# Kernel optimization log

Measured on AMD Instinct MI355X. Metric: run time of the kernel, lower is better.

Reference implementation:

```python
import jax, jax.numpy as jnp
import numpy as np

WH = WW = 7          # window size
N_TOK = WH * WW      # 49 tokens per window
HEADS = 8
HEAD_DIM = 32
DIM = HEADS * HEAD_DIM  # 256
NW = 64              # windows per image (56x56 / 7x7)
BW = 64 * NW         # batch_images * windows = 4096


def _rel_pos_index(wh, ww):
    # Swin-style relative position index, flattened to (N*N,)
    coords = np.stack(np.meshgrid(np.arange(wh), np.arange(ww), indexing='ij'))  # (2, wh, ww)
    coords = coords.reshape(2, -1)                                               # (2, N)
    rel = coords[:, :, None] - coords[:, None, :]                                # (2, N, N)
    rel = rel.transpose(1, 2, 0).astype(np.int64)                                # (N, N, 2)
    rel[:, :, 0] += wh - 1
    rel[:, :, 1] += ww - 1
    rel[:, :, 0] *= 2 * ww - 1
    return jnp.asarray(rel.sum(-1).reshape(-1))                                  # (N*N,)

_REL_IDX = _rel_pos_index(WH, WW)


def setup_inputs() -> dict:
    key = jax.random.key(0)
    ks = jax.random.split(key, 5)
    x = jax.random.normal(ks[0], (BW, N_TOK, DIM), dtype=jnp.float32)
    mask = jnp.zeros((1, NW, 1, N_TOK, N_TOK), dtype=jnp.float32)
    w_qkv = jax.random.normal(ks[1], (DIM, 3 * HEADS * HEAD_DIM), dtype=jnp.float32) * 0.02
    b_qkv = jnp.zeros((3 * HEADS * HEAD_DIM,), dtype=jnp.float32)
    rel_table = jax.random.normal(ks[2], ((2 * WH - 1) * (2 * WW - 1), HEADS), dtype=jnp.float32) * 0.02
    w_out = jax.random.normal(ks[3], (HEADS * HEAD_DIM, DIM), dtype=jnp.float32) * 0.02
    b_out = jnp.zeros((DIM,), dtype=jnp.float32)
    return {"x": x, "mask": mask, "w_qkv": w_qkv, "b_qkv": b_qkv,
            "rel_table": rel_table, "w_out": w_out, "b_out": b_out}


def reference(x, mask, w_qkv, b_qkv, rel_table, w_out, b_out):
    bw, n, d = x.shape
    # QKV projection then split per original Rearrange:
    # 'b n (qkv h hd) -> qkv b h n hd'
    qkv = (x @ w_qkv + b_qkv).reshape(bw, n, 3, HEADS, HEAD_DIM)
    qkv = qkv.transpose(2, 0, 3, 1, 4)  # (3, bw, h, n, hd)
    q, k, v = qkv[0], qkv[1], qkv[2]
    # NOTE: original computes einsum('bnid,bnjd->bnij', k, q): a[i,j] = k_i . q_j
    a = jnp.einsum('bhid,bhjd->bhij', k, q) / jnp.sqrt(jnp.asarray(HEAD_DIM, x.dtype))
    # relative position bias: table gather then '(i j) h -> h i j'
    bias = rel_table[_REL_IDX].reshape(n, n, HEADS).transpose(2, 0, 1)  # (h, n, n)
    a = a + bias
    # mask add: '(b nW) h i j -> b nW h i j', + mask, back
    nw = mask.shape[1]
    a = a.reshape(bw // nw, nw, HEADS, n, n) + mask
    a = a.reshape(bw, HEADS, n, n)
    a = jax.nn.softmax(a, axis=-1)
    y = jnp.einsum('bhij,bhjd->bhid', a, v)        # (bw, h, n, hd)
    y = y.transpose(0, 2, 1, 3).reshape(bw, n, HEADS * HEAD_DIM)
    return y @ w_out + b_out
```

## Files before the change

kernel.cpp:

```cpp
#include <hip/hip_runtime.h>

typedef __attribute__((ext_vector_type(8))) short short8;
typedef __attribute__((ext_vector_type(4))) float f32x4;
typedef unsigned short u16;

#define NTOK 49
#define NBLK 4096
#define LOG2E 1.4426950408889634f

#define XF 0
#define VY 16384
#define POOLN 32768

#define WS_WQT 0
#define WS_WOT 393216
#define WS_BIAS 524288
#define WS_MKG 655360

__device__ __forceinline__ u16 f2bf(float f) {
  unsigned u = __float_as_uint(f);
  return (u16)((u + 0x7fffu + ((u >> 16) & 1u)) >> 16);
}
__device__ __forceinline__ unsigned packbf(float a, float b) {
  unsigned r;
  asm("v_cvt_pk_bf16_f32 %0, %1, %2" : "=v"(r) : "v"(a), "v"(b));
  return r;
}

__device__ __forceinline__ short8 asm_frag(unsigned c0p0, unsigned c0p1,
                                           unsigned c1p0, unsigned c1p1,
                                           int srcA, int srcB, bool cSel) {
  unsigned a0 = (unsigned)__shfl((int)c0p0, srcA);
  unsigned b0 = (unsigned)__shfl((int)c1p0, srcA);
  unsigned a1 = (unsigned)__shfl((int)c0p1, srcA);
  unsigned b1 = (unsigned)__shfl((int)c1p1, srcA);
  unsigned a2 = (unsigned)__shfl((int)c0p0, srcB);
  unsigned b2 = (unsigned)__shfl((int)c1p0, srcB);
  unsigned a3 = (unsigned)__shfl((int)c0p1, srcB);
  unsigned b3 = (unsigned)__shfl((int)c1p1, srcB);
  union { unsigned u[4]; short8 s8; } r;
  r.u[0] = cSel ? b0 : a0;
  r.u[1] = cSel ? b1 : a1;
  r.u[2] = cSel ? b2 : a2;
  r.u[3] = cSel ? b3 : a3;
  return r.s8;
}

__global__ void prep_kernel(const float* __restrict__ w_qkv,
                            const float* __restrict__ w_out,
                            const float* __restrict__ rel,
                            const float* __restrict__ mask,
                            u16* __restrict__ wqTf,
                            u16* __restrict__ woTf,
                            float* __restrict__ biasf,
                            float* __restrict__ mkg) {
  const int stride = gridDim.x * blockDim.x;
  const int gid = blockIdx.x * blockDim.x + threadIdx.x;
  for (int e = gid; e < 48 * 8 * 64 * 8; e += stride) {
    int eL = e & 7, ln = (e >> 3) & 63, ks = (e >> 9) & 7, ctg = e >> 12;
    int k = ks * 32 + (ln >> 4) * 8 + eL;
    int c = ctg * 16 + (ln & 15);
    wqTf[e] = f2bf(w_qkv[k * 768 + c]);
  }
  for (int e = gid; e < 16 * 8 * 64 * 8; e += stride) {
    int eL = e & 7, ln = (e >> 3) & 63, ks = (e >> 9) & 7, ctg = e >> 12;
    int k = ks * 32 + (ln >> 4) * 8 + eL;
    int c = ctg * 16 + (ln & 15);
    woTf[e] = f2bf(w_out[k * 256 + c]);
  }
  for (int e = gid; e < 8 * 16 * 64 * 4; e += stride) {
    int rg = e & 3, ln = (e >> 2) & 63, t = (e >> 8) & 15, hh = e >> 12;
    int i = (t >> 2) * 16 + (ln & 15);
    int j = (t & 3) * 16 + (ln >> 4) * 4 + rg;
    float v;
    if (j >= NTOK) v = -1e30f;
    else if (i >= NTOK) v = 0.f;
    else {
      int dh = i / 7 - j / 7 + 6;
      int dw = i % 7 - j % 7 + 6;
      v = rel[(dh * 13 + dw) * 8 + hh];
    }
    biasf[e] = v * LOG2E;
  }
  for (int e = gid; e < 64 * 16 * 64 * 4; e += stride) {
    int rg = e & 3, ln = (e >> 2) & 63, t = (e >> 8) & 15, wdw = e >> 12;
    int i = (t >> 2) * 16 + (ln & 15);
    int j = (t & 3) * 16 + (ln >> 4) * 4 + rg;
    mkg[e] = (i < NTOK && j < NTOK) ? mask[wdw * (NTOK * NTOK) + i * NTOK + j] * LOG2E : 0.f;
  }
}

__global__ void __launch_bounds__(512, 2) winattn_mfma(
    const float* __restrict__ x,
    const float* __restrict__ b_qkv,
    const float* __restrict__ b_out,
    const u16* __restrict__ wqTf,
    const u16* __restrict__ woTf,
    const float* __restrict__ biasf,
    const float* __restrict__ mkg,
    float* __restrict__ out)
{
  __shared__ u16 pool[POOLN];
  const int b = blockIdx.x, tid = threadIdx.x;
  const int lane = tid & 63, lo = lane & 15, hi = lane >> 4;
  const int h = tid >> 6;
  const f32x4 zf = {0.f, 0.f, 0.f, 0.f};

  {
    const float4* xg = (const float4*)(x + (size_t)b * (NTOK * 256));
    for (int e = tid; e < 49 * 64; e += 512) {
      float4 v = xg[e];
      int r = e >> 6, c4 = (e & 63) << 2;
      int addr = (((r >> 4) * 8 + (c4 >> 5)) * 64 + ((c4 >> 3) & 3) * 16 + (r & 15)) * 8 + (c4 & 7);
      *(uint2*)&pool[XF + addr] = make_uint2(packbf(v.x, v.y), packbf(v.z, v.w));
    }
    if (tid < 15 * 64) {
      int e = tid;
      int r = 49 + (e >> 6), c4 = (e & 63) << 2;
      int addr = (((r >> 4) * 8 + (c4 >> 5)) * 64 + ((c4 >> 3) & 3) * 16 + (r & 15)) * 8 + (c4 & 7);
      *(uint2*)&pool[XF + addr] = make_uint2(0u, 0u);
    }
  }
  __syncthreads();

  const int srcA = lo + 32 * (hi & 1);
  const int srcB = srcA + 16;
  const bool cSel = (hi & 2) != 0;

  short8 qa[4], ka[4];
  {
    unsigned pq[2][4][2];
    {
      f32x4 acc[2][4];
      #pragma unroll
      for (int ct = 0; ct < 2; ++ct)
        #pragma unroll
        for (int rt = 0; rt < 4; ++rt) acc[ct][rt] = zf;
      #pragma unroll
      for (int ks = 0; ks < 8; ++ks) {
        short8 bx[4];
        #pragma unroll
        for (int rt = 0; rt < 4; ++rt)
          bx[rt] = *(const short8*)&pool[XF + ((rt * 8 + ks) * 64 + lane) * 8];
        short8 af0 = *(const short8*)&wqTf[((size_t)((2 * h) * 8 + ks) * 64 + lane) * 8];
        short8 af1 = *(const short8*)&wqTf[((size_t)((2 * h + 1) * 8 + ks) * 64 + lane) * 8];
        #pragma unroll
        for (int rt = 0; rt < 4; ++rt) {
          acc[0][rt] = __builtin_amdgcn_mfma_f32_16x16x32_bf16(af0, bx[rt], acc[0][rt], 0, 0, 0);
          acc[1][rt] = __builtin_amdgcn_mfma_f32_16x16x32_bf16(af1, bx[rt], acc[1][rt], 0, 0, 0);
        }
      }
      #pragma unroll
      for (int ct = 0; ct < 2; ++ct) {
        f32x4 bias = *(const f32x4*)(b_qkv + (2 * h + ct) * 16 + hi * 4);
        #pragma unroll
        for (int rt = 0; rt < 4; ++rt) {
          f32x4 v = acc[ct][rt] + bias;
          pq[ct][rt][0] = packbf(v[0], v[1]);
          pq[ct][rt][1] = packbf(v[2], v[3]);
        }
      }
    }
    {
      f32x4 acc[2][4];
      #pragma unroll
      for (int ct = 0; ct < 2; ++ct)
        #pragma unroll
        for (int rt = 0; rt < 4; ++rt) acc[ct][rt] = zf;
      #pragma unroll
      for (int ks = 0; ks < 8; ++ks) {
        short8 bx[4];
        #pragma unroll
        for (int rt = 0; rt < 4; ++rt)
          bx[rt] = *(const short8*)&pool[XF + ((rt * 8 + ks) * 64 + lane) * 8];
        short8 af0 = *(const short8*)&wqTf[((size_t)((16 + 2 * h) * 8 + ks) * 64 + lane) * 8];
        short8 af1 = *(const short8*)&wqTf[((size_t)((17 + 2 * h) * 8 + ks) * 64 + lane) * 8];
        #pragma unroll
        for (int rt = 0; rt < 4; ++rt) {
          acc[0][rt] = __builtin_amdgcn_mfma_f32_16x16x32_bf16(af0, bx[rt], acc[0][rt], 0, 0, 0);
          acc[1][rt] = __builtin_amdgcn_mfma_f32_16x16x32_bf16(af1, bx[rt], acc[1][rt], 0, 0, 0);
        }
      }
      unsigned pk[2][4][2];
      #pragma unroll
      for (int ct = 0; ct < 2; ++ct) {
        f32x4 bias = *(const f32x4*)(b_qkv + (16 + 2 * h + ct) * 16 + hi * 4);
        #pragma unroll
        for (int rt = 0; rt < 4; ++rt) {
          f32x4 v = acc[ct][rt] + bias;
          pk[ct][rt][0] = packbf(v[0], v[1]);
          pk[ct][rt][1] = packbf(v[2], v[3]);
        }
      }
      #pragma unroll
      for (int it = 0; it < 4; ++it)
        ka[it] = asm_frag(pk[0][it][0], pk[0][it][1], pk[1][it][0], pk[1][it][1],
                          srcA, srcB, cSel);
    }
    {
      f32x4 acc[2][4];
      #pragma unroll
      for (int ct = 0; ct < 2; ++ct)
        #pragma unroll
        for (int rt = 0; rt < 4; ++rt) acc[ct][rt] = zf;
      #pragma unroll
      for (int ks = 0; ks < 8; ++ks) {
        short8 bx[4];
        #pragma unroll
        for (int rt = 0; rt < 4; ++rt)
          bx[rt] = *(const short8*)&pool[XF + ((rt * 8 + ks) * 64 + lane) * 8];
        short8 af0 = *(const short8*)&wqTf[((size_t)((32 + 2 * h) * 8 + ks) * 64 + lane) * 8];
        short8 af1 = *(const short8*)&wqTf[((size_t)((33 + 2 * h) * 8 + ks) * 64 + lane) * 8];
        #pragma unroll
        for (int rt = 0; rt < 4; ++rt) {
          acc[0][rt] = __builtin_amdgcn_mfma_f32_16x16x32_bf16(bx[rt], af0, acc[0][rt], 0, 0, 0);
          acc[1][rt] = __builtin_amdgcn_mfma_f32_16x16x32_bf16(bx[rt], af1, acc[1][rt], 0, 0, 0);
        }
      }
      #pragma unroll
      for (int ct = 0; ct < 2; ++ct) {
        const float bv = b_qkv[(32 + 2 * h + ct) * 16 + lo];
        #pragma unroll
        for (int rt = 0; rt < 4; ++rt) {
          f32x4 v = acc[ct][rt];
          float v0 = v[0] + bv, v1 = v[1] + bv, v2 = v[2] + bv, v3 = v[3] + bv;
          int f = ct * 2 + (rt >> 1);
          int hiR = (rt & 1) * 2 + (hi >> 1);
          int eb = (hi & 1) * 4;
          *(uint2*)&pool[VY + (f * 8 + h) * 512 + (hiR * 16 + lo) * 8 + eb] =
              make_uint2(packbf(v0, v1), packbf(v2, v3));
        }
      }
    }
    #pragma unroll
    for (int jt = 0; jt < 4; ++jt)
      qa[jt] = asm_frag(pq[0][jt][0], pq[0][jt][1], pq[1][jt][0], pq[1][jt][1],
                        srcA, srcB, cSel);
  }
  __syncthreads();

  {
    short8 va[2][2];
    #pragma unroll
    for (int dblk = 0; dblk < 2; ++dblk)
      #pragma unroll
      for (int k2 = 0; k2 < 2; ++k2)
        va[dblk][k2] = *(const short8*)&pool[VY + ((dblk * 2 + k2) * 8 + h) * 512 + lane * 8];
    const float SC = 0.17677669529663687f * LOG2E;
    const float* bh = biasf + h * 4096;
    const float* mh = mkg + (size_t)(b & 63) * 4096;
    #pragma unroll
    for (int it = 0; it < 4; ++it) {
      float rs = 0.f;
      unsigned pit[4][2];
      #pragma unroll
      for (int jt = 0; jt < 4; ++jt) {
        f32x4 s = __builtin_amdgcn_mfma_f32_16x16x32_bf16(qa[jt], ka[it], zf, 0, 0, 0);
        const int t = it * 4 + jt;
        f32x4 bm = *(const f32x4*)&bh[(t * 64 + lane) * 4];
        f32x4 mm = *(const f32x4*)&mh[(t * 64 + lane) * 4];
        float p0 = exp2f(fmaf(s[0], SC, bm[0] + mm[0]));
        float p1 = exp2f(fmaf(s[1], SC, bm[1] + mm[1]));
        float p2 = exp2f(fmaf(s[2], SC, bm[2] + mm[2]));
        float p3 = exp2f(fmaf(s[3], SC, bm[3] + mm[3]));
        rs += (p0 + p1) + (p2 + p3);
        pit[jt][0] = packbf(p0, p1);
        pit[jt][1] = packbf(p2, p3);
      }
      float r2 = rs + __shfl_xor(rs, 16);
      const float inv = 1.f / (r2 + __shfl_xor(r2, 32));
      f32x4 ya0 = zf, ya1 = zf;
      #pragma unroll
      for (int k2 = 0; k2 < 2; ++k2) {
        short8 pb = asm_frag(pit[2 * k2][0], pit[2 * k2][1],
                             pit[2 * k2 + 1][0], pit[2 * k2 + 1][1], srcA, srcB, cSel);
        ya0 = __builtin_amdgcn_mfma_f32_16x16x32_bf16(va[0][k2], pb, ya0, 0, 0, 0);
        ya1 = __builtin_amdgcn_mfma_f32_16x16x32_bf16(va[1][k2], pb, ya1, 0, 0, 0);
      }
      #pragma unroll
      for (int dblk = 0; dblk < 2; ++dblk) {
        f32x4 yy = dblk ? ya1 : ya0;
        int hi2 = dblk * 2 + (hi >> 1);
        int eb = (hi & 1) * 4;
        *(uint2*)&pool[XF + ((it * 8 + h) * 64 + hi2 * 16 + lo) * 8 + eb] =
            make_uint2(packbf(yy[0] * inv, yy[1] * inv), packbf(yy[2] * inv, yy[3] * inv));
      }
    }
  }
  __syncthreads();

  {
    f32x4 pacc[2][4];
    #pragma unroll
    for (int ct = 0; ct < 2; ++ct)
      #pragma unroll
      for (int rt = 0; rt < 4; ++rt) pacc[ct][rt] = zf;
    #pragma unroll
    for (int ks = 0; ks < 8; ++ks) {
      short8 yb[4];
      #pragma unroll
      for (int rt = 0; rt < 4; ++rt)
        yb[rt] = *(const short8*)&pool[XF + ((rt * 8 + ks) * 64 + lane) * 8];
      #pragma unroll
      for (int ct = 0; ct < 2; ++ct) {
        short8 wf = *(const short8*)&woTf[((size_t)((h * 2 + ct) * 8 + ks) * 64 + lane) * 8];
        #pragma unroll
        for (int rt = 0; rt < 4; ++rt)
          pacc[ct][rt] = __builtin_amdgcn_mfma_f32_16x16x32_bf16(wf, yb[rt], pacc[ct][rt], 0, 0, 0);
      }
    }
    float* og = out + (size_t)b * (NTOK * 256);
    #pragma unroll
    for (int ct = 0; ct < 2; ++ct) {
      const int cb = (h * 2 + ct) * 16 + hi * 4;
      f32x4 bb = *(const f32x4*)(b_out + cb);
      #pragma unroll
      for (int rt = 0; rt < 4; ++rt) {
        const int r = rt * 16 + lo;
        if (r < NTOK) {
          f32x4 vv = pacc[ct][rt] + bb;
          *(f32x4*)(og + (size_t)r * 256 + cb) = vv;
        }
      }
    }
  }
}

extern "C" void kernel_launch(void* const* d_in, const int* in_sizes, int n_in,
                              void* d_out, int out_size, void* d_ws, size_t ws_size,
                              hipStream_t stream) {
  const float *x = nullptr, *mask = nullptr, *w_qkv = nullptr, *b_qkv = nullptr,
              *rel_t = nullptr, *w_out = nullptr, *b_out = nullptr;
  for (int i = 0; i < n_in; ++i) {
    const float* p = (const float*)d_in[i];
    switch (in_sizes[i]) {
      case 4096 * 49 * 256: x = p; break;
      case 64 * 49 * 49:    mask = p; break;
      case 256 * 768:       w_qkv = p; break;
      case 768:             b_qkv = p; break;
      case 169 * 8:         rel_t = p; break;
      case 256 * 256:       w_out = p; break;
      case 256:             b_out = p; break;
    }
  }
  char* wsb = (char*)d_ws;
  u16* wqTf    = (u16*)(wsb + WS_WQT);
  u16* woTf    = (u16*)(wsb + WS_WOT);
  float* biasf = (float*)(wsb + WS_BIAS);
  float* mkg   = (float*)(wsb + WS_MKG);

  hipLaunchKernelGGL(prep_kernel, dim3(1024), dim3(256), 0, stream,
                     w_qkv, w_out, rel_t, mask, wqTf, woTf, biasf, mkg);
  hipLaunchKernelGGL(winattn_mfma, dim3(NBLK), dim3(512), 0, stream,
                     x, b_qkv, b_out, wqTf, woTf, biasf, mkg, (float*)d_out);
}
```

Measured before the change: 343.3 us.

## Process two windows per 1024-thread block and route P through LDS

Each block now runs 1024 threads as two independent 512-thread groups, each handling one window with its own half of a doubled LDS pool. The launch bound changes from (512,2) to (1024,1), and the grid halves to 2048 blocks. The Q, K and V projections are restructured into separate top-level scopes, likely to cut live ranges. The P fragment for the PV matmul is now written to LDS and read back instead of being built in registers with asm_frag. That reuses the V region, which looks hazardous: V fragments are loaded into registers first, so a stale read may be fine, but the P writes and reads have no barrier within the wave. The extra LDS traffic and the tighter occupancy constraint could offset any gain.

```diff
diff --git a/kernel.cpp b/kernel.cpp
--- a/kernel.cpp
+++ b/kernel.cpp
@@ -5,12 +5,12 @@
 typedef unsigned short u16;
 
 #define NTOK 49
-#define NBLK 4096
 #define LOG2E 1.4426950408889634f
 
 #define XF 0
 #define VY 16384
-#define POOLN 32768
+#define GP 32768
+#define POOLN 65536
 
 #define WS_WQT 0
 #define WS_WOT 393216
@@ -90,7 +90,7 @@
   }
 }
 
-__global__ void __launch_bounds__(512, 2) winattn_mfma(
+__global__ void __launch_bounds__(1024, 1) winattn_mfma(
     const float* __restrict__ x,
     const float* __restrict__ b_qkv,
     const float* __restrict__ b_out,
@@ -101,24 +101,28 @@
     float* __restrict__ out)
 {
   __shared__ u16 pool[POOLN];
-  const int b = blockIdx.x, tid = threadIdx.x;
-  const int lane = tid & 63, lo = lane & 15, hi = lane >> 4;
-  const int h = tid >> 6;
+  const int tid = threadIdx.x;
+  const int g = tid >> 9;
+  const int gtid = tid & 511;
+  const int lane = gtid & 63, lo = lane & 15, hi = lane >> 4;
+  const int h = gtid >> 6;
+  const int b2 = blockIdx.x * 2 + g;
+  u16* gp = pool + g * GP;
   const f32x4 zf = {0.f, 0.f, 0.f, 0.f};
 
   {
-    const float4* xg = (const float4*)(x + (size_t)b * (NTOK * 256));
-    for (int e = tid; e < 49 * 64; e += 512) {
+    const float4* xg = (const float4*)(x + (size_t)b2 * (NTOK * 256));
+    for (int e = gtid; e < 49 * 64; e += 512) {
       float4 v = xg[e];
       int r = e >> 6, c4 = (e & 63) << 2;
       int addr = (((r >> 4) * 8 + (c4 >> 5)) * 64 + ((c4 >> 3) & 3) * 16 + (r & 15)) * 8 + (c4 & 7);
-      *(uint2*)&pool[XF + addr] = make_uint2(packbf(v.x, v.y), packbf(v.z, v.w));
-    }
-    if (tid < 15 * 64) {
-      int e = tid;
+      *(uint2*)&gp[XF + addr] = make_uint2(packbf(v.x, v.y), packbf(v.z, v.w));
+    }
+    if (gtid < 15 * 64) {
+      int e = gtid;
       int r = 49 + (e >> 6), c4 = (e & 63) << 2;
       int addr = (((r >> 4) * 8 + (c4 >> 5)) * 64 + ((c4 >> 3) & 3) * 16 + (r & 15)) * 8 + (c4 & 7);
-      *(uint2*)&pool[XF + addr] = make_uint2(0u, 0u);
+      *(uint2*)&gp[XF + addr] = make_uint2(0u, 0u);
     }
   }
   __syncthreads();
@@ -129,107 +133,34 @@
 
   short8 qa[4], ka[4];
   {
+    f32x4 acc[2][4];
+    #pragma unroll
+    for (int ct = 0; ct < 2; ++ct)
+      #pragma unroll
+      for (int rt = 0; rt < 4; ++rt) acc[ct][rt] = zf;
+    #pragma unroll
+    for (int ks = 0; ks < 8; ++ks) {
+      short8 bx[4];
+      #pragma unroll
+      for (int rt = 0; rt < 4; ++rt)
+        bx[rt] = *(const short8*)&gp[XF + ((rt * 8 + ks) * 64 + lane) * 8];
+      short8 af0 = *(const short8*)&wqTf[((size_t)((2 * h) * 8 + ks) * 64 + lane) * 8];
+      short8 af1 = *(const short8*)&wqTf[((size_t)((2 * h + 1) * 8 + ks) * 64 + lane) * 8];
+      #pragma unroll
+      for (int rt = 0; rt < 4; ++rt) {
+        acc[0][rt] = __builtin_amdgcn_mfma_f32_16x16x32_bf16(af0, bx[rt], acc[0][rt], 0, 0, 0);
+        acc[1][rt] = __builtin_amdgcn_mfma_f32_16x16x32_bf16(af1, bx[rt], acc[1][rt], 0, 0, 0);
+      }
+    }
     unsigned pq[2][4][2];
-    {
-      f32x4 acc[2][4];
-      #pragma unroll
-      for (int ct = 0; ct < 2; ++ct)
-        #pragma unroll
-        for (int rt = 0; rt < 4; ++rt) acc[ct][rt] = zf;
-      #pragma unroll
-      for (int ks = 0; ks < 8; ++ks) {
-        short8 bx[4];
-        #pragma unroll
-        for (int rt = 0; rt < 4; ++rt)
-          bx[rt] = *(const short8*)&pool[XF + ((rt * 8 + ks) * 64 + lane) * 8];
-        short8 af0 = *(const short8*)&wqTf[((size_t)((2 * h) * 8 + ks) * 64 + lane) * 8];
-        short8 af1 = *(const short8*)&wqTf[((size_t)((2 * h + 1) * 8 + ks) * 64 + lane) * 8];
-        #pragma unroll
-        for (int rt = 0; rt < 4; ++rt) {
-          acc[0][rt] = __builtin_amdgcn_mfma_f32_16x16x32_bf16(af0, bx[rt], acc[0][rt], 0, 0, 0);
-          acc[1][rt] = __builtin_amdgcn_mfma_f32_16x16x32_bf16(af1, bx[rt], acc[1][rt], 0, 0, 0);
-        }
-      }
-      #pragma unroll
-      for (int ct = 0; ct < 2; ++ct) {
-        f32x4 bias = *(const f32x4*)(b_qkv + (2 * h + ct) * 16 + hi * 4);
-        #pragma unroll
-        for (int rt = 0; rt < 4; ++rt) {
-          f32x4 v = acc[ct][rt] + bias;
-          pq[ct][rt][0] = packbf(v[0], v[1]);
-          pq[ct][rt][1] = packbf(v[2], v[3]);
-        }
-      }
-    }
-    {
-      f32x4 acc[2][4];
-      #pragma unroll
-      for (int ct = 0; ct < 2; ++ct)
-        #pragma unroll
-        for (int rt = 0; rt < 4; ++rt) acc[ct][rt] = zf;
-      #pragma unroll
-      for (int ks = 0; ks < 8; ++ks) {
-        short8 bx[4];
-        #pragma unroll
-        for (int rt = 0; rt < 4; ++rt)
-          bx[rt] = *(const short8*)&pool[XF + ((rt * 8 + ks) * 64 + lane) * 8];
-        short8 af0 = *(const short8*)&wqTf[((size_t)((16 + 2 * h) * 8 + ks) * 64 + lane) * 8];
-        short8 af1 = *(const short8*)&wqTf[((size_t)((17 + 2 * h) * 8 + ks) * 64 + lane) * 8];
-        #pragma unroll
-        for (int rt = 0; rt < 4; ++rt) {
-          acc[0][rt] = __builtin_amdgcn_mfma_f32_16x16x32_bf16(af0, bx[rt], acc[0][rt], 0, 0, 0);
-          acc[1][rt] = __builtin_amdgcn_mfma_f32_16x16x32_bf16(af1, bx[rt], acc[1][rt], 0, 0, 0);
-        }
-      }
-      unsigned pk[2][4][2];
-      #pragma unroll
-      for (int ct = 0; ct < 2; ++ct) {
-        f32x4 bias = *(const f32x4*)(b_qkv + (16 + 2 * h + ct) * 16 + hi * 4);
-        #pragma unroll
-        for (int rt = 0; rt < 4; ++rt) {
-          f32x4 v = acc[ct][rt] + bias;
-          pk[ct][rt][0] = packbf(v[0], v[1]);
-          pk[ct][rt][1] = packbf(v[2], v[3]);
-        }
-      }
-      #pragma unroll
-      for (int it = 0; it < 4; ++it)
-        ka[it] = asm_frag(pk[0][it][0], pk[0][it][1], pk[1][it][0], pk[1][it][1],
-                          srcA, srcB, cSel);
-    }
-    {
-      f32x4 acc[2][4];
-      #pragma unroll
-      for (int ct = 0; ct < 2; ++ct)
-        #pragma unroll
-        for (int rt = 0; rt < 4; ++rt) acc[ct][rt] = zf;
-      #pragma unroll
-      for (int ks = 0; ks < 8; ++ks) {
-        short8 bx[4];
-        #pragma unroll
-        for (int rt = 0; rt < 4; ++rt)
-          bx[rt] = *(const short8*)&pool[XF + ((rt * 8 + ks) * 64 + lane) * 8];
-        short8 af0 = *(const short8*)&wqTf[((size_t)((32 + 2 * h) * 8 + ks) * 64 + lane) * 8];
-        short8 af1 = *(const short8*)&wqTf[((size_t)((33 + 2 * h) * 8 + ks) * 64 + lane) * 8];
-        #pragma unroll
-        for (int rt = 0; rt < 4; ++rt) {
-          acc[0][rt] = __builtin_amdgcn_mfma_f32_16x16x32_bf16(bx[rt], af0, acc[0][rt], 0, 0, 0);
-          acc[1][rt] = __builtin_amdgcn_mfma_f32_16x16x32_bf16(bx[rt], af1, acc[1][rt], 0, 0, 0);
-        }
-      }
-      #pragma unroll
-      for (int ct = 0; ct < 2; ++ct) {
-        const float bv = b_qkv[(32 + 2 * h + ct) * 16 + lo];
-        #pragma unroll
-        for (int rt = 0; rt < 4; ++rt) {
-          f32x4 v = acc[ct][rt];
-          float v0 = v[0] + bv, v1 = v[1] + bv, v2 = v[2] + bv, v3 = v[3] + bv;
-          int f = ct * 2 + (rt >> 1);
-          int hiR = (rt & 1) * 2 + (hi >> 1);
-          int eb = (hi & 1) * 4;
-          *(uint2*)&pool[VY + (f * 8 + h) * 512 + (hiR * 16 + lo) * 8 + eb] =
-              make_uint2(packbf(v0, v1), packbf(v2, v3));
-        }
+    #pragma unroll
+    for (int ct = 0; ct < 2; ++ct) {
+      f32x4 bias = *(const f32x4*)(b_qkv + (2 * h + ct) * 16 + hi * 4);
+      #pragma unroll
+      for (int rt = 0; rt < 4; ++rt) {
+        f32x4 v = acc[ct][rt] + bias;
+        pq[ct][rt][0] = packbf(v[0], v[1]);
+        pq[ct][rt][1] = packbf(v[2], v[3]);
       }
     }
     #pragma unroll
@@ -237,6 +168,77 @@
       qa[jt] = asm_frag(pq[0][jt][0], pq[0][jt][1], pq[1][jt][0], pq[1][jt][1],
                         srcA, srcB, cSel);
   }
+  {
+    f32x4 acc[2][4];
+    #pragma unroll
+    for (int ct = 0; ct < 2; ++ct)
+      #pragma unroll
+      for (int rt = 0; rt < 4; ++rt) acc[ct][rt] = zf;
+    #pragma unroll
+    for (int ks = 0; ks < 8; ++ks) {
+      short8 bx[4];
+      #pragma unroll
+      for (int rt = 0; rt < 4; ++rt)
+        bx[rt] = *(const short8*)&gp[XF + ((rt * 8 + ks) * 64 + lane) * 8];
+      short8 af0 = *(const short8*)&wqTf[((size_t)((16 + 2 * h) * 8 + ks) * 64 + lane) * 8];
+      short8 af1 = *(const short8*)&wqTf[((size_t)((17 + 2 * h) * 8 + ks) * 64 + lane) * 8];
+      #pragma unroll
+      for (int rt = 0; rt < 4; ++rt) {
+        acc[0][rt] = __builtin_amdgcn_mfma_f32_16x16x32_bf16(af0, bx[rt], acc[0][rt], 0, 0, 0);
+        acc[1][rt] = __builtin_amdgcn_mfma_f32_16x16x32_bf16(af1, bx[rt], acc[1][rt], 0, 0, 0);
+      }
+    }
+    unsigned pk[2][4][2];
+    #pragma unroll
+    for (int ct = 0; ct < 2; ++ct) {
+      f32x4 bias = *(const f32x4*)(b_qkv + (16 + 2 * h + ct) * 16 + hi * 4);
+      #pragma unroll
+      for (int rt = 0; rt < 4; ++rt) {
+        f32x4 v = acc[ct][rt] + bias;
+        pk[ct][rt][0] = packbf(v[0], v[1]);
+        pk[ct][rt][1] = packbf(v[2], v[3]);
+      }
+    }
+    #pragma unroll
+    for (int it = 0; it < 4; ++it)
+      ka[it] = asm_frag(pk[0][it][0], pk[0][it][1], pk[1][it][0], pk[1][it][1],
+                        srcA, srcB, cSel);
+  }
+  {
+    f32x4 acc[2][4];
+    #pragma unroll
+    for (int ct = 0; ct < 2; ++ct)
+      #pragma unroll
+      for (int rt = 0; rt < 4; ++rt) acc[ct][rt] = zf;
+    #pragma unroll
+    for (int ks = 0; ks < 8; ++ks) {
+      short8 bx[4];
+      #pragma unroll
+      for (int rt = 0; rt < 4; ++rt)
+        bx[rt] = *(const short8*)&gp[XF + ((rt * 8 + ks) * 64 + lane) * 8];
+      short8 af0 = *(const short8*)&wqTf[((size_t)((32 + 2 * h) * 8 + ks) * 64 + lane) * 8];
+      short8 af1 = *(const short8*)&wqTf[((size_t)((33 + 2 * h) * 8 + ks) * 64 + lane) * 8];
+      #pragma unroll
+      for (int rt = 0; rt < 4; ++rt) {
+        acc[0][rt] = __builtin_amdgcn_mfma_f32_16x16x32_bf16(bx[rt], af0, acc[0][rt], 0, 0, 0);
+        acc[1][rt] = __builtin_amdgcn_mfma_f32_16x16x32_bf16(bx[rt], af1, acc[1][rt], 0, 0, 0);
+      }
+    }
+    #pragma unroll
+    for (int ct = 0; ct < 2; ++ct) {
+      const float bv = b_qkv[(32 + 2 * h + ct) * 16 + lo];
+      #pragma unroll
+      for (int rt = 0; rt < 4; ++rt) {
+        f32x4 v = acc[ct][rt];
+        float v0 = v[0] + bv, v1 = v[1] + bv, v2 = v[2] + bv, v3 = v[3] + bv;
+        int f = ct * 2 + (rt >> 1);
+        int hiR = (rt & 1) * 2 + (hi >> 1);
+        int eb = (hi & 1) * 4;
+        *(uint2*)&gp[VY + (f * 8 + h) * 512 + (hiR * 16 + lo) * 8 + eb] =
+            make_uint2(packbf(v0, v1), packbf(v2, v3));
+      }
+    }
+  }
   __syncthreads();
 
   {
@@ -245,10 +247,10 @@
     for (int dblk = 0; dblk < 2; ++dblk)
       #pragma unroll
       for (int k2 = 0; k2 < 2; ++k2)
-        va[dblk][k2] = *(const short8*)&pool[VY + ((dblk * 2 + k2) * 8 + h) * 512 + lane * 8];
+        va[dblk][k2] = *(const short8*)&gp[VY + ((dblk * 2 + k2) * 8 + h) * 512 + lane * 8];
     const float SC = 0.17677669529663687f * LOG2E;
     const float* bh = biasf + h * 4096;
-    const float* mh = mkg + (size_t)(b & 63) * 4096;
+    const float* mh = mkg + (size_t)(b2 & 63) * 4096;
     #pragma unroll
     for (int it = 0; it < 4; ++it) {
       float rs = 0.f;
@@ -267,13 +269,20 @@
         pit[jt][0] = packbf(p0, p1);
         pit[jt][1] = packbf(p2, p3);
       }
+      #pragma unroll
+      for (int jt = 0; jt < 4; ++jt) {
+        int k2 = jt >> 1;
+        int hi2 = (jt & 1) * 2 + (hi >> 1);
+        int eb = (hi & 1) * 4;
+        *(uint2*)&gp[VY + (k2 * 8 + h) * 512 + (hi2 * 16 + lo) * 8 + eb] =
+            make_uint2(pit[jt][0], pit[jt][1]);
+      }
       float r2 = rs + __shfl_xor(rs, 16);
       const float inv = 1.f / (r2 + __shfl_xor(r2, 32));
       f32x4 ya0 = zf, ya1 = zf;
       #pragma unroll
       for (int k2 = 0; k2 < 2; ++k2) {
-        short8 pb = asm_frag(pit[2 * k2][0], pit[2 * k2][1],
-                             pit[2 * k2 + 1][0], pit[2 * k2 + 1][1], srcA, srcB, cSel);
+        short8 pb = *(const short8*)&gp[VY + (k2 * 8 + h) * 512 + lane * 8];
         ya0 = __builtin_amdgcn_mfma_f32_16x16x32_bf16(va[0][k2], pb, ya0, 0, 0, 0);
         ya1 = __builtin_amdgcn_mfma_f32_16x16x32_bf16(va[1][k2], pb, ya1, 0, 0, 0);
       }
@@ -282,7 +291,7 @@
         f32x4 yy = dblk ? ya1 : ya0;
         int hi2 = dblk * 2 + (hi >> 1);
         int eb = (hi & 1) * 4;
-        *(uint2*)&pool[XF + ((it * 8 + h) * 64 + hi2 * 16 + lo) * 8 + eb] =
+        *(uint2*)&gp[XF + ((it * 8 + h) * 64 + hi2 * 16 + lo) * 8 + eb] =
             make_uint2(packbf(yy[0] * inv, yy[1] * inv), packbf(yy[2] * inv, yy[3] * inv));
       }
     }
@@ -300,7 +309,7 @@
       short8 yb[4];
       #pragma unroll
       for (int rt = 0; rt < 4; ++rt)
-        yb[rt] = *(const short8*)&pool[XF + ((rt * 8 + ks) * 64 + lane) * 8];
+        yb[rt] = *(const short8*)&gp[XF + ((rt * 8 + ks) * 64 + lane) * 8];
       #pragma unroll
       for (int ct = 0; ct < 2; ++ct) {
         short8 wf = *(const short8*)&woTf[((size_t)((h * 2 + ct) * 8 + ks) * 64 + lane) * 8];
@@ -309,7 +318,7 @@
           pacc[ct][rt] = __builtin_amdgcn_mfma_f32_16x16x32_bf16(wf, yb[rt], pacc[ct][rt], 0, 0, 0);
       }
     }
-    float* og = out + (size_t)b * (NTOK * 256);
+    float* og = out + (size_t)b2 * (NTOK * 256);
     #pragma unroll
     for (int ct = 0; ct < 2; ++ct) {
       const int cb = (h * 2 + ct) * 16 + hi * 4;
@@ -351,6 +360,6 @@
 
   hipLaunchKernelGGL(prep_kernel, dim3(1024), dim3(256), 0, stream,
                      w_qkv, w_out, rel_t, mask, wqTf, woTf, biasf, mkg);
-  hipLaunchKernelGGL(winattn_mfma, dim3(NBLK), dim3(512), 0, stream,
+  hipLaunchKernelGGL(winattn_mfma, dim3(2048), dim3(1024), 0, stream,
                      x, b_qkv, b_out, wqTf, woTf, biasf, mkg, (float*)d_out);
 }
```

Measured after the change: 646.9 us. 88.4% more time.

## Fold softmax scale into Q weights, precombine bias+mask, use LDS for fragment transposes

Applied to the files above, without the earlier changes.

Pre-scales the Q projection weights and bias by 1/sqrt(d)*log2e so the score FMA becomes a plain add. An extra prep kernel builds a combined per-window, per-head bias+mask table (8 MB), so each score tile needs one global load instead of two. The shuffle-based fragment transposes for Q, K and P are replaced with LDS round-trips, and the Y layout in LDS is changed. This trades cross-lane shuffles for LDS traffic and adds one syncthreads, a larger combined table that must stay cached, and a launch that depends on workspace size.

```diff
diff --git a/kernel.cpp b/kernel.cpp
--- a/kernel.cpp
+++ b/kernel.cpp
@@ -14,8 +14,11 @@
 
 #define WS_WQT 0
 #define WS_WOT 393216
-#define WS_BIAS 524288
-#define WS_MKG 655360
+#define WS_BQS 524288
+#define WS_BIAS 528384
+#define WS_MKG 659456
+#define WS_CMB 1708032
+#define WS_NEED (WS_CMB + 8388608)
 
 __device__ __forceinline__ u16 f2bf(float f) {
   unsigned u = __float_as_uint(f);
@@ -27,40 +30,26 @@
   return r;
 }
 
-__device__ __forceinline__ short8 asm_frag(unsigned c0p0, unsigned c0p1,
-                                           unsigned c1p0, unsigned c1p1,
-                                           int srcA, int srcB, bool cSel) {
-  unsigned a0 = (unsigned)__shfl((int)c0p0, srcA);
-  unsigned b0 = (unsigned)__shfl((int)c1p0, srcA);
-  unsigned a1 = (unsigned)__shfl((int)c0p1, srcA);
-  unsigned b1 = (unsigned)__shfl((int)c1p1, srcA);
-  unsigned a2 = (unsigned)__shfl((int)c0p0, srcB);
-  unsigned b2 = (unsigned)__shfl((int)c1p0, srcB);
-  unsigned a3 = (unsigned)__shfl((int)c0p1, srcB);
-  unsigned b3 = (unsigned)__shfl((int)c1p1, srcB);
-  union { unsigned u[4]; short8 s8; } r;
-  r.u[0] = cSel ? b0 : a0;
-  r.u[1] = cSel ? b1 : a1;
-  r.u[2] = cSel ? b2 : a2;
-  r.u[3] = cSel ? b3 : a3;
-  return r.s8;
-}
-
 __global__ void prep_kernel(const float* __restrict__ w_qkv,
                             const float* __restrict__ w_out,
                             const float* __restrict__ rel,
                             const float* __restrict__ mask,
+                            const float* __restrict__ b_qkv,
                             u16* __restrict__ wqTf,
                             u16* __restrict__ woTf,
+                            float* __restrict__ bqs,
                             float* __restrict__ biasf,
                             float* __restrict__ mkg) {
+  const float SCQ = 0.17677669529663687f * LOG2E;
   const int stride = gridDim.x * blockDim.x;
   const int gid = blockIdx.x * blockDim.x + threadIdx.x;
   for (int e = gid; e < 48 * 8 * 64 * 8; e += stride) {
     int eL = e & 7, ln = (e >> 3) & 63, ks = (e >> 9) & 7, ctg = e >> 12;
     int k = ks * 32 + (ln >> 4) * 8 + eL;
     int c = ctg * 16 + (ln & 15);
-    wqTf[e] = f2bf(w_qkv[k * 768 + c]);
+    float wv = w_qkv[k * 768 + c];
+    if (ctg < 16) wv *= SCQ;
+    wqTf[e] = f2bf(wv);
   }
   for (int e = gid; e < 16 * 8 * 64 * 8; e += stride) {
     int eL = e & 7, ln = (e >> 3) & 63, ks = (e >> 9) & 7, ctg = e >> 12;
@@ -68,6 +57,8 @@
     int c = ctg * 16 + (ln & 15);
     woTf[e] = f2bf(w_out[k * 256 + c]);
   }
+  for (int e = gid; e < 768; e += stride)
+    bqs[e] = b_qkv[e] * (e < 256 ? SCQ : 1.f);
   for (int e = gid; e < 8 * 16 * 64 * 4; e += stride) {
     int rg = e & 3, ln = (e >> 2) & 63, t = (e >> 8) & 15, hh = e >> 12;
     int i = (t >> 2) * 16 + (ln & 15);
@@ -90,14 +81,25 @@
   }
 }
 
+__global__ void prep2_kernel(const float* __restrict__ biasf,
+                             const float* __restrict__ mkg,
+                             float* __restrict__ cmb) {
+  const int stride = gridDim.x * blockDim.x;
+  for (int e = blockIdx.x * blockDim.x + threadIdx.x; e < 64 * 8 * 4096; e += stride) {
+    int x = e & 4095, hh = (e >> 12) & 7, wdw = e >> 15;
+    cmb[e] = biasf[hh * 4096 + x] + mkg[wdw * 4096 + x];
+  }
+}
+
 __global__ void __launch_bounds__(512, 2) winattn_mfma(
     const float* __restrict__ x,
-    const float* __restrict__ b_qkv,
+    const float* __restrict__ bqs,
     const float* __restrict__ b_out,
     const u16* __restrict__ wqTf,
     const u16* __restrict__ woTf,
     const float* __restrict__ biasf,
     const float* __restrict__ mkg,
+    const float* __restrict__ cmb,
     float* __restrict__ out)
 {
   __shared__ u16 pool[POOLN];
@@ -114,8 +116,7 @@
       int addr = (((r >> 4) * 8 + (c4 >> 5)) * 64 + ((c4 >> 3) & 3) * 16 + (r & 15)) * 8 + (c4 & 7);
       *(uint2*)&pool[XF + addr] = make_uint2(packbf(v.x, v.y), packbf(v.z, v.w));
     }
-    if (tid < 15 * 64) {
-      int e = tid;
+    for (int e = tid; e < 15 * 64; e += 512) {
       int r = 49 + (e >> 6), c4 = (e & 63) << 2;
       int addr = (((r >> 4) * 8 + (c4 >> 5)) * 64 + ((c4 >> 3) & 3) * 16 + (r & 15)) * 8 + (c4 & 7);
       *(uint2*)&pool[XF + addr] = make_uint2(0u, 0u);
@@ -123,103 +124,52 @@
   }
   __syncthreads();
 
-  const int srcA = lo + 32 * (hi & 1);
-  const int srcB = srcA + 16;
-  const bool cSel = (hi & 2) != 0;
-
-  short8 qa[4], ka[4];
-  {
-    unsigned pq[2][4][2];
-    {
-      f32x4 acc[2][4];
-      #pragma unroll
-      for (int ct = 0; ct < 2; ++ct)
-        #pragma unroll
-        for (int rt = 0; rt < 4; ++rt) acc[ct][rt] = zf;
-      #pragma unroll
-      for (int ks = 0; ks < 8; ++ks) {
-        short8 bx[4];
-        #pragma unroll
-        for (int rt = 0; rt < 4; ++rt)
-          bx[rt] = *(const short8*)&pool[XF + ((rt * 8 + ks) * 64 + lane) * 8];
-        short8 af0 = *(const short8*)&wqTf[((size_t)((2 * h) * 8 + ks) * 64 + lane) * 8];
-        short8 af1 = *(const short8*)&wqTf[((size_t)((2 * h + 1) * 8 + ks) * 64 + lane) * 8];
+  unsigned pq[2][4][2], pk[2][4][2];
+  #pragma unroll
+  for (int pass = 0; pass < 3; ++pass) {
+    const int c0 = (pass == 0) ? 2 * h : (pass == 1 ? 16 + 2 * h : 32 + 2 * h);
+    f32x4 acc[2][4];
+    #pragma unroll
+    for (int ct = 0; ct < 2; ++ct)
+      #pragma unroll
+      for (int rt = 0; rt < 4; ++rt) acc[ct][rt] = zf;
+    #pragma unroll
+    for (int ks = 0; ks < 8; ++ks) {
+      short8 bx[4];
+      #pragma unroll
+      for (int rt = 0; rt < 4; ++rt)
+        bx[rt] = *(const short8*)&pool[XF + ((rt * 8 + ks) * 64 + lane) * 8];
+      short8 af0 = *(const short8*)&wqTf[((size_t)((c0 + 0) * 8 + ks) * 64 + lane) * 8];
+      short8 af1 = *(const short8*)&wqTf[((size_t)((c0 + 1) * 8 + ks) * 64 + lane) * 8];
+      if (pass < 2) {
         #pragma unroll
         for (int rt = 0; rt < 4; ++rt) {
           acc[0][rt] = __builtin_amdgcn_mfma_f32_16x16x32_bf16(af0, bx[rt], acc[0][rt], 0, 0, 0);
           acc[1][rt] = __builtin_amdgcn_mfma_f32_16x16x32_bf16(af1, bx[rt], acc[1][rt], 0, 0, 0);
         }
-      }
-      #pragma unroll
-      for (int ct = 0; ct < 2; ++ct) {
-        f32x4 bias = *(const f32x4*)(b_qkv + (2 * h + ct) * 16 + hi * 4);
-        #pragma unroll
-        for (int rt = 0; rt < 4; ++rt) {
-          f32x4 v = acc[ct][rt] + bias;
-          pq[ct][rt][0] = packbf(v[0], v[1]);
-          pq[ct][rt][1] = packbf(v[2], v[3]);
-        }
-      }
-    }
-    {
-      f32x4 acc[2][4];
-      #pragma unroll
-      for (int ct = 0; ct < 2; ++ct)
-        #pragma unroll
-        for (int rt = 0; rt < 4; ++rt) acc[ct][rt] = zf;
-      #pragma unroll
-      for (int ks = 0; ks < 8; ++ks) {
-        short8 bx[4];
-        #pragma unroll
-        for (int rt = 0; rt < 4; ++rt)
-          bx[rt] = *(const short8*)&pool[XF + ((rt * 8 + ks) * 64 + lane) * 8];
-        short8 af0 = *(const short8*)&wqTf[((size_t)((16 + 2 * h) * 8 + ks) * 64 + lane) * 8];
-        short8 af1 = *(const short8*)&wqTf[((size_t)((17 + 2 * h) * 8 + ks) * 64 + lane) * 8];
-        #pragma unroll
-        for (int rt = 0; rt < 4; ++rt) {
-          acc[0][rt] = __builtin_amdgcn_mfma_f32_16x16x32_bf16(af0, bx[rt], acc[0][rt], 0, 0, 0);
-          acc[1][rt] = __builtin_amdgcn_mfma_f32_16x16x32_bf16(af1, bx[rt], acc[1][rt], 0, 0, 0);
-        }
-      }
-      unsigned pk[2][4][2];
-      #pragma unroll
-      for (int ct = 0; ct < 2; ++ct) {
-        f32x4 bias = *(const f32x4*)(b_qkv + (16 + 2 * h + ct) * 16 + hi * 4);
-        #pragma unroll
-        for (int rt = 0; rt < 4; ++rt) {
-          f32x4 v = acc[ct][rt] + bias;
-          pk[ct][rt][0] = packbf(v[0], v[1]);
-          pk[ct][rt][1] = packbf(v[2], v[3]);
-        }
-      }
-      #pragma unroll
-      for (int it = 0; it < 4; ++it)
-        ka[it] = asm_frag(pk[0][it][0], pk[0][it][1], pk[1][it][0], pk[1][it][1],
-                          srcA, srcB, cSel);
-    }
-    {
-      f32x4 acc[2][4];
-      #pragma unroll
-      for (int ct = 0; ct < 2; ++ct)
-        #pragma unroll
-        for (int rt = 0; rt < 4; ++rt) acc[ct][rt] = zf;
-      #pragma unroll
-      for (int ks = 0; ks < 8; ++ks) {
-        short8 bx[4];
-        #pragma unroll
-        for (int rt = 0; rt < 4; ++rt)
-          bx[rt] = *(const short8*)&pool[XF + ((rt * 8 + ks) * 64 + lane) * 8];
-        short8 af0 = *(const short8*)&wqTf[((size_t)((32 + 2 * h) * 8 + ks) * 64 + lane) * 8];
-        short8 af1 = *(const short8*)&wqTf[((size_t)((33 + 2 * h) * 8 + ks) * 64 + lane) * 8];
+      } else {
         #pragma unroll
         for (int rt = 0; rt < 4; ++rt) {
           acc[0][rt] = __builtin_amdgcn_mfma_f32_16x16x32_bf16(bx[rt], af0, acc[0][rt], 0, 0, 0);
           acc[1][rt] = __builtin_amdgcn_mfma_f32_16x16x32_bf16(bx[rt], af1, acc[1][rt], 0, 0, 0);
         }
       }
+    }
+    if (pass < 2) {
       #pragma unroll
       for (int ct = 0; ct < 2; ++ct) {
-        const float bv = b_qkv[(32 + 2 * h + ct) * 16 + lo];
+        f32x4 bias = *(const f32x4*)(bqs + (c0 + ct) * 16 + hi * 4);
+        #pragma unroll
+        for (int rt = 0; rt < 4; ++rt) {
+          f32x4 v = acc[ct][rt] + bias;
+          if (pass == 0) { pq[ct][rt][0] = packbf(v[0], v[1]); pq[ct][rt][1] = packbf(v[2], v[3]); }
+          else           { pk[ct][rt][0] = packbf(v[0], v[1]); pk[ct][rt][1] = packbf(v[2], v[3]); }
+        }
+      }
+    } else {
+      #pragma unroll
+      for (int ct = 0; ct < 2; ++ct) {
+        const float bv = bqs[(c0 + ct) * 16 + lo];
         #pragma unroll
         for (int rt = 0; rt < 4; ++rt) {
           f32x4 v = acc[ct][rt];
@@ -232,12 +182,37 @@
         }
       }
     }
+  }
+  __syncthreads();
+
+  short8 qa[4], ka[4];
+  {
+    u16* slice = pool + XF + h * 2048;
+    #pragma unroll
+    for (int ct = 0; ct < 2; ++ct)
+      #pragma unroll
+      for (int rt = 0; rt < 4; ++rt) {
+        int hi2 = ct * 2 + (hi >> 1);
+        int eb = (hi & 1) * 4;
+        *(uint2*)&slice[(rt * 64 + hi2 * 16 + lo) * 8 + eb] =
+            make_uint2(pq[ct][rt][0], pq[ct][rt][1]);
+      }
     #pragma unroll
     for (int jt = 0; jt < 4; ++jt)
-      qa[jt] = asm_frag(pq[0][jt][0], pq[0][jt][1], pq[1][jt][0], pq[1][jt][1],
-                        srcA, srcB, cSel);
-  }
-  __syncthreads();
+      qa[jt] = *(const short8*)&slice[(jt * 64 + lane) * 8];
+    #pragma unroll
+    for (int ct = 0; ct < 2; ++ct)
+      #pragma unroll
+      for (int rt = 0; rt < 4; ++rt) {
+        int hi2 = ct * 2 + (hi >> 1);
+        int eb = (hi & 1) * 4;
+        *(uint2*)&slice[(rt * 64 + hi2 * 16 + lo) * 8 + eb] =
+            make_uint2(pk[ct][rt][0], pk[ct][rt][1]);
+      }
+    #pragma unroll
+    for (int it = 0; it < 4; ++it)
+      ka[it] = *(const short8*)&slice[(it * 64 + lane) * 8];
+  }
 
   {
     short8 va[2][2];
@@ -246,34 +221,43 @@
       #pragma unroll
       for (int k2 = 0; k2 < 2; ++k2)
         va[dblk][k2] = *(const short8*)&pool[VY + ((dblk * 2 + k2) * 8 + h) * 512 + lane * 8];
-    const float SC = 0.17677669529663687f * LOG2E;
-    const float* bh = biasf + h * 4096;
-    const float* mh = mkg + (size_t)(b & 63) * 4096;
+    const float* cb;
+    const float* mb = nullptr;
+    if (cmb) {
+      cb = cmb + (((size_t)(b & 63) * 8 + h) << 12);
+    } else {
+      cb = biasf + h * 4096;
+      mb = mkg + (size_t)(b & 63) * 4096;
+    }
     #pragma unroll
     for (int it = 0; it < 4; ++it) {
       float rs = 0.f;
-      unsigned pit[4][2];
       #pragma unroll
       for (int jt = 0; jt < 4; ++jt) {
         f32x4 s = __builtin_amdgcn_mfma_f32_16x16x32_bf16(qa[jt], ka[it], zf, 0, 0, 0);
         const int t = it * 4 + jt;
-        f32x4 bm = *(const f32x4*)&bh[(t * 64 + lane) * 4];
-        f32x4 mm = *(const f32x4*)&mh[(t * 64 + lane) * 4];
-        float p0 = exp2f(fmaf(s[0], SC, bm[0] + mm[0]));
-        float p1 = exp2f(fmaf(s[1], SC, bm[1] + mm[1]));
-        float p2 = exp2f(fmaf(s[2], SC, bm[2] + mm[2]));
-        float p3 = exp2f(fmaf(s[3], SC, bm[3] + mm[3]));
+        f32x4 c4 = *(const f32x4*)&cb[(t * 64 + lane) * 4];
+        if (mb) {
+          f32x4 m4 = *(const f32x4*)&mb[(t * 64 + lane) * 4];
+          c4[0] += m4[0]; c4[1] += m4[1]; c4[2] += m4[2]; c4[3] += m4[3];
+        }
+        float p0 = exp2f(s[0] + c4[0]);
+        float p1 = exp2f(s[1] + c4[1]);
+        float p2 = exp2f(s[2] + c4[2]);
+        float p3 = exp2f(s[3] + c4[3]);
         rs += (p0 + p1) + (p2 + p3);
-        pit[jt][0] = packbf(p0, p1);
-        pit[jt][1] = packbf(p2, p3);
+        int k2 = jt >> 1;
+        int hi2 = (jt & 1) * 2 + (hi >> 1);
+        int eb = (hi & 1) * 4;
+        *(uint2*)&pool[VY + (k2 * 8 + h) * 512 + (hi2 * 16 + lo) * 8 + eb] =
+            make_uint2(packbf(p0, p1), packbf(p2, p3));
       }
       float r2 = rs + __shfl_xor(rs, 16);
       const float inv = 1.f / (r2 + __shfl_xor(r2, 32));
       f32x4 ya0 = zf, ya1 = zf;
       #pragma unroll
       for (int k2 = 0; k2 < 2; ++k2) {
-        short8 pb = asm_frag(pit[2 * k2][0], pit[2 * k2][1],
-                             pit[2 * k2 + 1][0], pit[2 * k2 + 1][1], srcA, srcB, cSel);
+        short8 pb = *(const short8*)&pool[VY + (k2 * 8 + h) * 512 + lane * 8];
         ya0 = __builtin_amdgcn_mfma_f32_16x16x32_bf16(va[0][k2], pb, ya0, 0, 0, 0);
         ya1 = __builtin_amdgcn_mfma_f32_16x16x32_bf16(va[1][k2], pb, ya1, 0, 0, 0);
       }
@@ -282,7 +266,7 @@
         f32x4 yy = dblk ? ya1 : ya0;
         int hi2 = dblk * 2 + (hi >> 1);
         int eb = (hi & 1) * 4;
-        *(uint2*)&pool[XF + ((it * 8 + h) * 64 + hi2 * 16 + lo) * 8 + eb] =
+        *(uint2*)&pool[XF + (h * 4 + it) * 512 + (hi2 * 16 + lo) * 8 + eb] =
             make_uint2(packbf(yy[0] * inv, yy[1] * inv), packbf(yy[2] * inv, yy[3] * inv));
       }
     }
@@ -300,7 +284,7 @@
       short8 yb[4];
       #pragma unroll
       for (int rt = 0; rt < 4; ++rt)
-        yb[rt] = *(const short8*)&pool[XF + ((rt * 8 + ks) * 64 + lane) * 8];
+        yb[rt] = *(const short8*)&pool[XF + (ks * 4 + rt) * 512 + lane * 8];
       #pragma unroll
       for (int ct = 0; ct < 2; ++ct) {
         short8 wf = *(const short8*)&woTf[((size_t)((h * 2 + ct) * 8 + ks) * 64 + lane) * 8];
@@ -312,14 +296,14 @@
     float* og = out + (size_t)b * (NTOK * 256);
     #pragma unroll
     for (int ct = 0; ct < 2; ++ct) {
-      const int cb = (h * 2 + ct) * 16 + hi * 4;
-      f32x4 bb = *(const f32x4*)(b_out + cb);
+      const int cb2 = (h * 2 + ct) * 16 + hi * 4;
+      f32x4 bb = *(const f32x4*)(b_out + cb2);
       #pragma unroll
       for (int rt = 0; rt < 4; ++rt) {
         const int r = rt * 16 + lo;
         if (r < NTOK) {
           f32x4 vv = pacc[ct][rt] + bb;
-          *(f32x4*)(og + (size_t)r * 256 + cb) = vv;
+          *(f32x4*)(og + (size_t)r * 256 + cb2) = vv;
         }
       }
     }
@@ -346,11 +330,18 @@
   char* wsb = (char*)d_ws;
   u16* wqTf    = (u16*)(wsb + WS_WQT);
   u16* woTf    = (u16*)(wsb + WS_WOT);
+  float* bqs   = (float*)(wsb + WS_BQS);
   float* biasf = (float*)(wsb + WS_BIAS);
   float* mkg   = (float*)(wsb + WS_MKG);
+  const bool fits = (ws_size >= (size_t)WS_NEED);
+  float* cmb   = fits ? (float*)(wsb + WS_CMB) : nullptr;
 
   hipLaunchKernelGGL(prep_kernel, dim3(1024), dim3(256), 0, stream,
-                     w_qkv, w_out, rel_t, mask, wqTf, woTf, biasf, mkg);
+                     w_qkv, w_out, rel_t, mask, b_qkv, wqTf, woTf, bqs, biasf, mkg);
+  if (fits) {
+    hipLaunchKernelGGL(prep2_kernel, dim3(2048), dim3(256), 0, stream,
+                       biasf, mkg, cmb);
+  }
   hipLaunchKernelGGL(winattn_mfma, dim3(NBLK), dim3(512), 0, stream,
-                     x, b_qkv, b_out, wqTf, woTf, biasf, mkg, (float*)d_out);
-}
+                     x, bqs, b_out, wqTf, woTf, biasf, mkg, cmb, (float*)d_out);
+}
```

After: 320.5 us. 6.6% less time.
